# Kernel tuning notes

Measured on AMD Instinct MI355X. Metric: run time of the kernel, lower is better.

The kernel has to match this reference:

```python
import jax, jax.numpy as jnp
import numpy as np

N = 50000      # nodes
E = 800000     # edges (avg degree 16)
D_IN = 64
D_H = 64


def setup_inputs() -> dict:
    key = jax.random.key(0)
    k = jax.random.split(key, 4)
    x = jax.random.normal(k[0], (N, D_IN), dtype=jnp.float32)
    edge_index = jax.random.randint(k[1], (2, E), 0, N, dtype=jnp.int64)
    W1 = jax.random.normal(k[2], (D_IN, D_H), dtype=jnp.float32) * (1.0 / np.sqrt(D_IN))
    b1 = jnp.zeros((D_H,), dtype=jnp.float32)
    W2 = jax.random.normal(k[3], (D_H, 1), dtype=jnp.float32) * (1.0 / np.sqrt(D_H))
    b2 = jnp.zeros((1,), dtype=jnp.float32)
    return {"x": x, "edge_index": edge_index, "W1": W1, "b1": b1, "W2": W2, "b2": b2}


def gcn_conv(x, src, dst, W, b):
    """PyG-style GCNConv: linear -> symmetric-normalized scatter-aggregate + bias.
    src/dst already include self-loops."""
    n = x.shape[0]
    h = x @ W                                                   # [N, Dout]
    deg = jax.ops.segment_sum(jnp.ones_like(dst, dtype=h.dtype), dst, num_segments=n)
    dinv_sqrt = jnp.where(deg > 0, jax.lax.rsqrt(jnp.maximum(deg, 1e-12)), 0.0)
    norm = dinv_sqrt[src] * dinv_sqrt[dst]                       # [E+N]
    agg = jax.ops.segment_sum(h[src] * norm[:, None], dst, num_segments=n)
    return agg + b


def reference(x, edge_index, W1, b1, W2, b2):
    n = x.shape[0]
    loops = jnp.arange(n, dtype=edge_index.dtype)
    src = jnp.concatenate([edge_index[0], loops])                # add self-loops
    dst = jnp.concatenate([edge_index[1], loops])
    h = jax.nn.relu(gcn_conv(x, src, dst, W1, b1))               # [N, D_H]
    out = gcn_conv(h, src, dst, W2, b2)                          # [N, 1]
    return out.squeeze(-1)                                       # [N]
```

## Files before the change

### kernel.cpp

```cpp
#include <hip/hip_runtime.h>
#include <hip/hip_fp16.h>

#define D 64
#define PW2 128
#define PSH2 7
#define EPB 2048

__global__ __launch_bounds__(512) void k_hist(const int* __restrict__ dst, int E,
                                              int* __restrict__ counts, int NP) {
    extern __shared__ int lh[];
    int t = threadIdx.x, b = blockIdx.x;
    for (int i = t; i < NP; i += 512) lh[i] = 0;
    __syncthreads();
    int base = b * EPB;
#pragma unroll
    for (int k = 0; k < EPB / 512; ++k) {
        int e = base + k * 512 + t;
        if (e < E) atomicAdd(&lh[dst[e] >> PSH2], 1);
    }
    __syncthreads();
    for (int i = t; i < NP; i += 512) counts[(size_t)b * NP + i] = lh[i];
}

__global__ __launch_bounds__(512) void k_scanA(int* __restrict__ counts, int NB, int NP,
                                               int* __restrict__ bin_total) {
    __shared__ int sh[512];
    int t = threadIdx.x, bin = blockIdx.x;
    int v = (t < NB) ? counts[(size_t)t * NP + bin] : 0;
    sh[t] = v;
    __syncthreads();
    for (int off = 1; off < 512; off <<= 1) {
        int u = (t >= off) ? sh[t - off] : 0;
        __syncthreads();
        sh[t] += u;
        __syncthreads();
    }
    if (t < NB) counts[(size_t)t * NP + bin] = sh[t] - v;
    if (t == 511) bin_total[bin] = sh[511];
}

__global__ __launch_bounds__(1024) void k_scanB(const int* __restrict__ bin_total, int NP,
                                                int* __restrict__ bin_base) {
    __shared__ int sh[1024];
    int t = threadIdx.x;
    int i0 = 2 * t, i1 = 2 * t + 1;
    int v0 = (i0 < NP) ? bin_total[i0] : 0;
    int v1 = (i1 < NP) ? bin_total[i1] : 0;
    int s = v0 + v1;
    sh[t] = s;
    __syncthreads();
    for (int off = 1; off < 1024; off <<= 1) {
        int u = (t >= off) ? sh[t - off] : 0;
        __syncthreads();
        sh[t] += u;
        __syncthreads();
    }
    int excl = sh[t] - s;
    if (i0 < NP) bin_base[i0] = excl;
    if (i1 < NP) bin_base[i1] = excl + v0;
    if (t == 1023) bin_base[NP] = sh[1023];
}

__global__ __launch_bounds__(512) void k_scatter(const int* __restrict__ src,
        const int* __restrict__ dst, int E, const int* __restrict__ counts,
        const int* __restrict__ bin_base, int NP, int* __restrict__ csr_e) {
    extern __shared__ int cur[];
    int t = threadIdx.x, b = blockIdx.x;
    for (int i = t; i < NP; i += 512)
        cur[i] = counts[(size_t)b * NP + i] + bin_base[i];
    __syncthreads();
    int base = b * EPB;
#pragma unroll
    for (int k = 0; k < EPB / 512; ++k) {
        int e = base + k * 512 + t;
        if (e < E) {
            int s = src[e], d = dst[e];
            int pos = atomicAdd(&cur[d >> PSH2], 1);
            csr_e[pos] = s | ((d & (PW2 - 1)) << 16);
        }
    }
}

__global__ __launch_bounds__(512) void k_sort2(const int* __restrict__ csr_e,
        const int* __restrict__ bin_base, int n,
        int* __restrict__ csr_src, int* __restrict__ row_ptr,
        float* __restrict__ dinv) {
    __shared__ int cnt[PW2];
    __shared__ int sh[512];
    __shared__ int cursor[PW2];
    int t = threadIdx.x, p = blockIdx.x;
    int beg = bin_base[p], end = bin_base[p + 1];
    if (t < PW2) cnt[t] = 0;
    __syncthreads();
    for (int i = beg + t; i < end; i += 512) atomicAdd(&cnt[csr_e[i] >> 16], 1);
    __syncthreads();
    int val = (t < PW2) ? cnt[t] : 0;
    sh[t] = val;
    __syncthreads();
    for (int off = 1; off < 512; off <<= 1) {
        int u = (t >= off) ? sh[t - off] : 0;
        __syncthreads();
        sh[t] += u;
        __syncthreads();
    }
    int excl = sh[t] - val;
    if (t < PW2) {
        cursor[t] = beg + excl;
        int node = p * PW2 + t;
        if (node <= n) {
            row_ptr[node] = beg + excl;
            if (node < n) dinv[node] = rsqrtf((float)(val + 1));
        }
    }
    __syncthreads();
    for (int i = beg + t; i < end; i += 512) {
        int e = csr_e[i];
        int q = atomicAdd(&cursor[e >> 16], 1);
        csr_src[q] = e & 0xFFFF;
    }
}

#define NPW 16
__global__ __launch_bounds__(256) void k_zw(
        const float* __restrict__ x, const float* __restrict__ dinv,
        const float* __restrict__ W1, __half* __restrict__ zh, int n) {
    __shared__ float lrow[4][D];
    int tid = threadIdx.x;
    int wave = tid >> 6, lane = tid & 63;
    float w1c[D];
#pragma unroll
    for (int d = 0; d < D; ++d) w1c[d] = W1[d * D + lane];
    int v0 = (blockIdx.x * 4 + wave) * NPW;
    for (int k = 0; k < NPW; ++k) {
        int v = v0 + k;
        if (v >= n) break;
        lrow[wave][lane] = x[(size_t)v * D + lane];
        __builtin_amdgcn_wave_barrier();
        float h = 0.0f;
#pragma unroll
        for (int db = 0; db < D; db += 4) {
            float4 r = *(const float4*)&lrow[wave][db];
            h = fmaf(r.x, w1c[db], h);
            h = fmaf(r.y, w1c[db + 1], h);
            h = fmaf(r.z, w1c[db + 2], h);
            h = fmaf(r.w, w1c[db + 3], h);
        }
        zh[(size_t)v * D + lane] = __float2half(h * dinv[v]);
        __builtin_amdgcn_wave_barrier();
    }
}

__global__ __launch_bounds__(256) void k_gather(
        const __half2* __restrict__ zh, const float* __restrict__ dinv,
        const int* __restrict__ row_ptr, const int* __restrict__ csr_src,
        const float* __restrict__ b1, const float* __restrict__ W2,
        float* __restrict__ sd, int n) {
    int tid = threadIdx.x;
    int wave = tid >> 6, lane = tid & 63;
    int eg = lane >> 3, dg = lane & 7;
    int v = blockIdx.x * 4 + wave;
    if (v >= n) return;
    float dv = dinv[v];
    int beg = row_ptr[v], end = row_ptr[v + 1];

    float4 A = make_float4(0.f, 0.f, 0.f, 0.f);
    float4 B = make_float4(0.f, 0.f, 0.f, 0.f);
    float2 f;
#define ACC16(r)                                                        \
    {   __half2 h0 = *(__half2*)&(r).x, h1 = *(__half2*)&(r).y,         \
                h2 = *(__half2*)&(r).z, h3 = *(__half2*)&(r).w;         \
        f = __half22float2(h0); A.x += f.x; A.y += f.y;                 \
        f = __half22float2(h1); A.z += f.x; A.w += f.y;                 \
        f = __half22float2(h2); B.x += f.x; B.y += f.y;                 \
        f = __half22float2(h3); B.z += f.x; B.w += f.y; }

    if (eg == 0) {
        int4 r = *(const int4*)(zh + (size_t)v * 32 + dg * 4);
        ACC16(r);
    }
    int base = beg;
    for (; base + 16 <= end; base += 16) {
        int u0 = csr_src[base + eg];
        int u1 = csr_src[base + 8 + eg];
        int4 r0 = *(const int4*)(zh + (size_t)u0 * 32 + dg * 4);
        int4 r1 = *(const int4*)(zh + (size_t)u1 * 32 + dg * 4);
        ACC16(r0);
        ACC16(r1);
    }
    for (; base < end; base += 8) {
        int idx = base + eg;
        if (idx < end) {
            int u = csr_src[idx];
            int4 r = *(const int4*)(zh + (size_t)u * 32 + dg * 4);
            ACC16(r);
        }
    }
#undef ACC16
#pragma unroll
    for (int off = 8; off <= 32; off <<= 1) {
        A.x += __shfl_xor(A.x, off, 64); A.y += __shfl_xor(A.y, off, 64);
        A.z += __shfl_xor(A.z, off, 64); A.w += __shfl_xor(A.w, off, 64);
        B.x += __shfl_xor(B.x, off, 64); B.y += __shfl_xor(B.y, off, 64);
        B.z += __shfl_xor(B.z, off, 64); B.w += __shfl_xor(B.w, off, 64);
    }
    float4 b1a = *(const float4*)&b1[dg * 8];
    float4 b1b = *(const float4*)&b1[dg * 8 + 4];
    float4 w2a = *(const float4*)&W2[dg * 8];
    float4 w2b = *(const float4*)&W2[dg * 8 + 4];
    float part;
    part  = fmaxf(fmaf(dv, A.x, b1a.x), 0.f) * w2a.x;
    part += fmaxf(fmaf(dv, A.y, b1a.y), 0.f) * w2a.y;
    part += fmaxf(fmaf(dv, A.z, b1a.z), 0.f) * w2a.z;
    part += fmaxf(fmaf(dv, A.w, b1a.w), 0.f) * w2a.w;
    part += fmaxf(fmaf(dv, B.x, b1b.x), 0.f) * w2b.x;
    part += fmaxf(fmaf(dv, B.y, b1b.y), 0.f) * w2b.y;
    part += fmaxf(fmaf(dv, B.z, b1b.z), 0.f) * w2b.z;
    part += fmaxf(fmaf(dv, B.w, b1b.w), 0.f) * w2b.w;
    part += __shfl_xor(part, 1, 64);
    part += __shfl_xor(part, 2, 64);
    part += __shfl_xor(part, 4, 64);
    if (lane == 0) sd[v] = part * dv;
}

__global__ __launch_bounds__(256) void k_out(const float* __restrict__ sd,
        const float* __restrict__ dinv, const int* __restrict__ row_ptr,
        const int* __restrict__ csr_src, const float* __restrict__ b2,
        float* __restrict__ out, int n) {
    int t = blockIdx.x * blockDim.x + threadIdx.x;
    int v = t >> 3, r = t & 7;
    if (v >= n) return;
    int beg = row_ptr[v], end = row_ptr[v + 1];
    float a = (r == 0) ? sd[v] : 0.0f;
    for (int i = beg + r; i < end; i += 8) a += sd[csr_src[i]];
    a += __shfl_xor(a, 1, 64);
    a += __shfl_xor(a, 2, 64);
    a += __shfl_xor(a, 4, 64);
    if (r == 0) out[v] = b2[0] + a * dinv[v];
}

extern "C" void kernel_launch(void* const* d_in, const int* in_sizes, int n_in,
                              void* d_out, int out_size, void* d_ws, size_t ws_size,
                              hipStream_t stream) {
    const float* x  = (const float*)d_in[0];
    const int*   ei = (const int*)d_in[1];
    const float* W1 = (const float*)d_in[2];
    const float* b1 = (const float*)d_in[3];
    const float* W2 = (const float*)d_in[4];
    const float* b2 = (const float*)d_in[5];

    int n = in_sizes[0] / D;
    int E = in_sizes[1] / 2;
    const int* src = ei;
    const int* dst = ei + E;

    int NP = (n + PW2 - 1) / PW2;
    int NB = (E + EPB - 1) / EPB;

    char* ws = (char*)d_ws;
    auto take = [&](size_t bytes) {
        char* p = ws;
        ws += (bytes + 255) & ~(size_t)255;
        return p;
    };
    int*     counts    = (int*)take((size_t)NB * NP * sizeof(int));
    int*     bin_total = (int*)take((size_t)NP * sizeof(int));
    int*     bin_base  = (int*)take((size_t)(NP + 1) * sizeof(int));
    int*     csr_e     = (int*)take((size_t)E * sizeof(int));
    int*     csr_src   = (int*)take((size_t)E * sizeof(int));
    int*     row_ptr   = (int*)take((size_t)(n + 1) * sizeof(int));
    float*   dinv      = (float*)take((size_t)n * sizeof(float));
    float*   sd        = (float*)take((size_t)n * sizeof(float));
    __half*  zh        = (__half*)take((size_t)n * D * sizeof(__half));

    float* out = (float*)d_out;
    size_t ldsNP = (size_t)NP * sizeof(int);

    k_hist<<<NB, 512, ldsNP, stream>>>(dst, E, counts, NP);
    k_scanA<<<NP, 512, 0, stream>>>(counts, NB, NP, bin_total);
    k_scanB<<<1, 1024, 0, stream>>>(bin_total, NP, bin_base);
    k_scatter<<<NB, 512, ldsNP, stream>>>(src, dst, E, counts, bin_base, NP, csr_e);
    k_sort2<<<NP, 512, 0, stream>>>(csr_e, bin_base, n, csr_src, row_ptr, dinv);

    k_zw<<<(n + 4 * NPW - 1) / (4 * NPW), 256, 0, stream>>>(x, dinv, W1, zh, n);

    k_gather<<<(n + 3) / 4, 256, 0, stream>>>((const __half2*)zh, dinv, row_ptr,
                                              csr_src, b1, W2, sd, n);
    k_out<<<((size_t)n * 8 + 255) / 256, 256, 0, stream>>>(sd, dinv, row_ptr, csr_src,
                                                           b2, out, n);
}
```

Measured before the change: 81.29 us.

## Drop global bin scan kernel and fuse feature transform into per-bin sort

Removes the single-block k_scanB launch. Each k_scatter and k_sort2 block now redundantly scans the bin totals in shared memory to get its own bin offsets. The x@W1 scaled-by-dinv transform is folded into the per-bin sort kernel, reusing the degree normalisation kept in shared memory. This cuts two kernel launches and their serialization gaps, at the cost of repeated small scans per block. It also assumes at most 512 bins, since the in-block scan covers only 512 entries.

```diff
diff --git a/kernel.cpp b/kernel.cpp
--- a/kernel.cpp
+++ b/kernel.cpp
@@ -39,35 +39,26 @@
     if (t == 511) bin_total[bin] = sh[511];
 }
 
-__global__ __launch_bounds__(1024) void k_scanB(const int* __restrict__ bin_total, int NP,
-                                                int* __restrict__ bin_base) {
-    __shared__ int sh[1024];
-    int t = threadIdx.x;
-    int i0 = 2 * t, i1 = 2 * t + 1;
-    int v0 = (i0 < NP) ? bin_total[i0] : 0;
-    int v1 = (i1 < NP) ? bin_total[i1] : 0;
-    int s = v0 + v1;
-    sh[t] = s;
-    __syncthreads();
-    for (int off = 1; off < 1024; off <<= 1) {
-        int u = (t >= off) ? sh[t - off] : 0;
-        __syncthreads();
-        sh[t] += u;
-        __syncthreads();
-    }
-    int excl = sh[t] - s;
-    if (i0 < NP) bin_base[i0] = excl;
-    if (i1 < NP) bin_base[i1] = excl + v0;
-    if (t == 1023) bin_base[NP] = sh[1023];
-}
-
 __global__ __launch_bounds__(512) void k_scatter(const int* __restrict__ src,
         const int* __restrict__ dst, int E, const int* __restrict__ counts,
-        const int* __restrict__ bin_base, int NP, int* __restrict__ csr_e) {
+        const int* __restrict__ bin_total, int NP, int* __restrict__ csr_e) {
+    __shared__ int sh[512];
+    __shared__ int bb[512];
     extern __shared__ int cur[];
     int t = threadIdx.x, b = blockIdx.x;
+    int v = (t < NP) ? bin_total[t] : 0;
+    sh[t] = v;
+    __syncthreads();
+    for (int off = 1; off < 512; off <<= 1) {
+        int u = (t >= off) ? sh[t - off] : 0;
+        __syncthreads();
+        sh[t] += u;
+        __syncthreads();
+    }
+    bb[t] = sh[t] - v;
+    __syncthreads();
     for (int i = t; i < NP; i += 512)
-        cur[i] = counts[(size_t)b * NP + i] + bin_base[i];
+        cur[i] = counts[(size_t)b * NP + i] + bb[i];
     __syncthreads();
     int base = b * EPB;
 #pragma unroll
@@ -81,17 +72,33 @@
     }
 }
 
-__global__ __launch_bounds__(512) void k_sort2(const int* __restrict__ csr_e,
-        const int* __restrict__ bin_base, int n,
+__global__ __launch_bounds__(512) void k_sort2zw(const int* __restrict__ csr_e,
+        const int* __restrict__ bin_total, int NP, int n,
+        const float* __restrict__ x, const float* __restrict__ W1,
         int* __restrict__ csr_src, int* __restrict__ row_ptr,
-        float* __restrict__ dinv) {
+        float* __restrict__ dinv, __half* __restrict__ zh) {
+    __shared__ int sh[512];
     __shared__ int cnt[PW2];
-    __shared__ int sh[512];
     __shared__ int cursor[PW2];
+    __shared__ float ldv[PW2];
+    __shared__ float lrow[8][D];
+    __shared__ int s_beg, s_end;
     int t = threadIdx.x, p = blockIdx.x;
-    int beg = bin_base[p], end = bin_base[p + 1];
+
+    int bv = (t < NP) ? bin_total[t] : 0;
+    sh[t] = bv;
+    __syncthreads();
+    for (int off = 1; off < 512; off <<= 1) {
+        int u = (t >= off) ? sh[t - off] : 0;
+        __syncthreads();
+        sh[t] += u;
+        __syncthreads();
+    }
+    if (t == p) { s_beg = sh[t] - bv; s_end = sh[t]; }
     if (t < PW2) cnt[t] = 0;
     __syncthreads();
+    int beg = s_beg, end = s_end;
+
     for (int i = beg + t; i < end; i += 512) atomicAdd(&cnt[csr_e[i] >> 16], 1);
     __syncthreads();
     int val = (t < PW2) ? cnt[t] : 0;
@@ -107,9 +114,11 @@
     if (t < PW2) {
         cursor[t] = beg + excl;
         int node = p * PW2 + t;
+        float dv = rsqrtf((float)(val + 1));
+        ldv[t] = dv;
         if (node <= n) {
             row_ptr[node] = beg + excl;
-            if (node < n) dinv[node] = rsqrtf((float)(val + 1));
+            if (node < n) dinv[node] = dv;
         }
     }
     __syncthreads();
@@ -118,34 +127,28 @@
         int q = atomicAdd(&cursor[e >> 16], 1);
         csr_src[q] = e & 0xFFFF;
     }
-}
-
-#define NPW 16
-__global__ __launch_bounds__(256) void k_zw(
-        const float* __restrict__ x, const float* __restrict__ dinv,
-        const float* __restrict__ W1, __half* __restrict__ zh, int n) {
-    __shared__ float lrow[4][D];
-    int tid = threadIdx.x;
-    int wave = tid >> 6, lane = tid & 63;
+
+    int wave = t >> 6, lane = t & 63;
     float w1c[D];
 #pragma unroll
     for (int d = 0; d < D; ++d) w1c[d] = W1[d * D + lane];
-    int v0 = (blockIdx.x * 4 + wave) * NPW;
-    for (int k = 0; k < NPW; ++k) {
-        int v = v0 + k;
-        if (v >= n) break;
-        lrow[wave][lane] = x[(size_t)v * D + lane];
+    int r0 = wave * 16;
+    for (int k = 0; k < 16; ++k) {
+        int r = r0 + k;
+        int node = p * PW2 + r;
+        if (node >= n) break;
+        lrow[wave][lane] = x[(size_t)node * D + lane];
         __builtin_amdgcn_wave_barrier();
         float h = 0.0f;
 #pragma unroll
         for (int db = 0; db < D; db += 4) {
-            float4 r = *(const float4*)&lrow[wave][db];
-            h = fmaf(r.x, w1c[db], h);
-            h = fmaf(r.y, w1c[db + 1], h);
-            h = fmaf(r.z, w1c[db + 2], h);
-            h = fmaf(r.w, w1c[db + 3], h);
-        }
-        zh[(size_t)v * D + lane] = __float2half(h * dinv[v]);
+            float4 rr = *(const float4*)&lrow[wave][db];
+            h = fmaf(rr.x, w1c[db], h);
+            h = fmaf(rr.y, w1c[db + 1], h);
+            h = fmaf(rr.z, w1c[db + 2], h);
+            h = fmaf(rr.w, w1c[db + 3], h);
+        }
+        zh[(size_t)node * D + lane] = __float2half(h * ldv[r]);
         __builtin_amdgcn_wave_barrier();
     }
 }
@@ -264,7 +267,6 @@
     };
     int*     counts    = (int*)take((size_t)NB * NP * sizeof(int));
     int*     bin_total = (int*)take((size_t)NP * sizeof(int));
-    int*     bin_base  = (int*)take((size_t)(NP + 1) * sizeof(int));
     int*     csr_e     = (int*)take((size_t)E * sizeof(int));
     int*     csr_src   = (int*)take((size_t)E * sizeof(int));
     int*     row_ptr   = (int*)take((size_t)(n + 1) * sizeof(int));
@@ -277,11 +279,9 @@
 
     k_hist<<<NB, 512, ldsNP, stream>>>(dst, E, counts, NP);
     k_scanA<<<NP, 512, 0, stream>>>(counts, NB, NP, bin_total);
-    k_scanB<<<1, 1024, 0, stream>>>(bin_total, NP, bin_base);
-    k_scatter<<<NB, 512, ldsNP, stream>>>(src, dst, E, counts, bin_base, NP, csr_e);
-    k_sort2<<<NP, 512, 0, stream>>>(csr_e, bin_base, n, csr_src, row_ptr, dinv);
-
-    k_zw<<<(n + 4 * NPW - 1) / (4 * NPW), 256, 0, stream>>>(x, dinv, W1, zh, n);
+    k_scatter<<<NB, 512, ldsNP, stream>>>(src, dst, E, counts, bin_total, NP, csr_e);
+    k_sort2zw<<<NP, 512, 0, stream>>>(csr_e, bin_total, NP, n, x, W1,
+                                      csr_src, row_ptr, dinv, zh);
 
     k_gather<<<(n + 3) / 4, 256, 0, stream>>>((const __half2*)zh, dinv, row_ptr,
                                               csr_src, b1, W2, sd, n);
```

Result: faster. 77.27 us (-4.9%).
